# Optimization experiments

Measured on AMD Instinct MI355X. Metric: run time of the kernel, lower is better.

## Reference

```python
import jax, jax.numpy as jnp
import numpy as np

D_IN, L, D, K, N_CLASSES = 1024, 512, 384, 1, 2

def setup_inputs() -> dict:
    key = jax.random.key(0)
    ks = jax.random.split(key, 11)
    x = jax.random.normal(ks[0], (2, 40000, D_IN), dtype=jnp.float32)
    # Linear params stored as [in, out]; xavier-normal-ish scale
    def w(k, i, o):
        return jax.random.normal(k, (i, o), dtype=jnp.float32) * jnp.sqrt(2.0 / (i + o))
    return {
        "x": x,
        "Wf": w(ks[1], D_IN, L), "bf": jnp.zeros((L,), jnp.float32),
        "Wa": w(ks[2], L, D),    "ba": jnp.zeros((D,), jnp.float32),
        "Wb": w(ks[3], L, D),    "bb": jnp.zeros((D,), jnp.float32),
        "Wc": w(ks[4], D, K),    "bc": jnp.zeros((K,), jnp.float32),
        "Wcls": w(ks[5], L * K, N_CLASSES), "bcls": jnp.zeros((N_CLASSES,), jnp.float32),
    }

def reference(x, Wf, bf, Wa, ba, Wb, bb, Wc, bc, Wcls, bcls):
    # feature embed: Linear + ReLU  (mil_norm=None -> Identity norms)
    h = jax.nn.relu(jnp.einsum('bnd,de->bne', x, Wf) + bf)   # [B,N,L]
    # gated attention
    a = jnp.tanh(jnp.einsum('bnl,ld->bnd', h, Wa) + ba)      # [B,N,D]
    g = jax.nn.sigmoid(jnp.einsum('bnl,ld->bnd', h, Wb) + bb)
    s = jnp.einsum('bnd,dk->bnk', a * g, Wc) + bc            # [B,N,K]
    A = jax.nn.softmax(jnp.swapaxes(s, -1, -2), axis=-1)     # [B,K,N]
    pooled = jnp.einsum('bkn,bnl->bkl', A, h)                # [B,K,L]
    logits = jnp.squeeze(pooled, 1) @ Wcls + bcls            # [B,n_classes]
    return logits
```

## Files before the change

kernel.cpp:

```cpp
#include <hip/hip_runtime.h>
#include <cstdint>

typedef _Float16 f16;
typedef __attribute__((ext_vector_type(8))) _Float16 half8;
typedef __attribute__((ext_vector_type(4))) float floatx4;

#define NB      40000
#define M_TOTAL 80000
#define DIN     1024
#define LDIM    512
#define DDIM    384

__global__ void k_prep(const float* __restrict__ Wf, const float* __restrict__ Wa,
                       const float* __restrict__ Wb,
                       f16* __restrict__ packedF, f16* __restrict__ packedAB)
{
    const int gid = blockIdx.x * 256 + threadIdx.x;
    if (gid < 65536) {
        const int lq = gid & 3, n = (gid >> 2) & 511, kb = gid >> 11;
        const int kbase = kb * 32 + lq * 8;
        half8 v;
        #pragma unroll
        for (int j = 0; j < 8; ++j) v[j] = (f16)Wf[(kbase + j) * 512 + n];
        *(half8*)&packedF[(long)gid * 8] = v;
    } else if (gid < 65536 + 49152) {
        const int g = gid - 65536;
        const int kb = g / 3072;
        const int rem = g - kb * 3072;
        const int c = rem >> 2, lq = rem & 3;
        const int d = ((c >> 5) << 4) + (c & 15);
        const int type = (c >> 4) & 1;
        const float* src = type ? Wb : Wa;
        const int kbase = kb * 32 + lq * 8;
        half8 v;
        #pragma unroll
        for (int j = 0; j < 8; ++j) v[j] = (f16)src[(kbase + j) * 384 + d];
        *(half8*)&packedAB[(long)g * 8] = v;
    }
}

__global__ __launch_bounds__(512, 4) void k_gemm1(
    const float* __restrict__ x, const f16* __restrict__ packedF,
    const float* __restrict__ bf, f16* __restrict__ h)
{
    __shared__ __align__(16) f16 As[2][64][72];
    const int tid = threadIdx.x;
    const int w = tid >> 6, lane = tid & 63, lr = lane & 15, lq = lane >> 4;
    const long row0 = (long)blockIdx.x * 64;
    const int sr = tid >> 3, sk = (tid & 7) * 8;
    const float* xp = x + (row0 + sr) * DIN + sk;

    floatx4 acc[4][4] = {};

    float4 xa = *(const float4*)xp;
    float4 xb = *(const float4*)(xp + 4);
    {
        half8 hv;
        hv[0]=(f16)xa.x; hv[1]=(f16)xa.y; hv[2]=(f16)xa.z; hv[3]=(f16)xa.w;
        hv[4]=(f16)xb.x; hv[5]=(f16)xb.y; hv[6]=(f16)xb.z; hv[7]=(f16)xb.w;
        *(half8*)&As[0][sr][sk] = hv;
    }
    for (int kt = 0; kt < 16; ++kt) {
        __syncthreads();
        const int cur = kt & 1;
        if (kt < 15) {
            const float* q = xp + (kt + 1) * 64;
            xa = *(const float4*)q;
            xb = *(const float4*)(q + 4);
        }
        #pragma unroll
        for (int kq = 0; kq < 2; ++kq) {
            const int kb = kt * 2 + kq;
            half8 bfr[4];
            #pragma unroll
            for (int tj = 0; tj < 4; ++tj)
                bfr[tj] = *(const half8*)&packedF[(long)((kb * 512 + w * 64 + tj * 16 + lr) << 5) + lq * 8];
            half8 af[4];
            #pragma unroll
            for (int ti = 0; ti < 4; ++ti)
                af[ti] = *(const half8*)&As[cur][ti * 16 + lr][kq * 32 + lq * 8];
            #pragma unroll
            for (int tj = 0; tj < 4; ++tj)
                #pragma unroll
                for (int ti = 0; ti < 4; ++ti)
                    acc[ti][tj] = __builtin_amdgcn_mfma_f32_16x16x32_f16(af[ti], bfr[tj], acc[ti][tj], 0, 0, 0);
        }
        if (kt < 15) {
            half8 hv;
            hv[0]=(f16)xa.x; hv[1]=(f16)xa.y; hv[2]=(f16)xa.z; hv[3]=(f16)xa.w;
            hv[4]=(f16)xb.x; hv[5]=(f16)xb.y; hv[6]=(f16)xb.z; hv[7]=(f16)xb.w;
            *(half8*)&As[cur ^ 1][sr][sk] = hv;
        }
    }
    #pragma unroll
    for (int tj = 0; tj < 4; ++tj) {
        const int col = w * 64 + tj * 16 + lr;
        const float bias = bf[col];
        #pragma unroll
        for (int ti = 0; ti < 4; ++ti) {
            const long rbase = row0 + ti * 16 + lq * 4;
            #pragma unroll
            for (int r = 0; r < 4; ++r) {
                float v = fmaxf(acc[ti][tj][r] + bias, 0.0f);
                h[(rbase + r) * LDIM + col] = (f16)v;
            }
        }
    }
}

__device__ inline float fast_sigmoid(float xx) { return 1.0f / (1.0f + __expf(-xx)); }
__device__ inline float fast_tanh(float xx) {
    float e = __expf(-2.0f * fabsf(xx));
    float r = (1.0f - e) / (1.0f + e);
    return xx >= 0.0f ? r : -r;
}

__global__ __launch_bounds__(512, 2) void k_gemm2(
    const f16* __restrict__ h, const f16* __restrict__ packedAB,
    const float* __restrict__ ba, const float* __restrict__ bb,
    const float* __restrict__ Wc, float* __restrict__ s)
{
    __shared__ __align__(16) f16 Hs[2][64][136];
    const int tid = threadIdx.x;
    const int w = tid >> 6, lane = tid & 63, lr = lane & 15, lq = lane >> 4;
    const long row0 = (long)blockIdx.x * 64;
    const int sr = tid >> 3, sk = (tid & 7) * 16;
    const f16* hp = h + (row0 + sr) * LDIM + sk;

    floatx4 acc[4][6] = {};

    half8 s0 = *(const half8*)hp;
    half8 s1 = *(const half8*)(hp + 8);
    *(half8*)&Hs[0][sr][sk]     = s0;
    *(half8*)&Hs[0][sr][sk + 8] = s1;

    for (int kt = 0; kt < 4; ++kt) {
        __syncthreads();
        const int cur = kt & 1;
        if (kt < 3) {
            const f16* q = hp + (kt + 1) * 128;
            s0 = *(const half8*)q;
            s1 = *(const half8*)(q + 8);
        }
        #pragma unroll
        for (int kq = 0; kq < 4; ++kq) {
            const int kb = kt * 4 + kq;
            half8 af[4];
            #pragma unroll
            for (int ti = 0; ti < 4; ++ti)
                af[ti] = *(const half8*)&Hs[cur][ti * 16 + lr][kq * 32 + lq * 8];
            #pragma unroll
            for (int tj = 0; tj < 6; ++tj) {
                half8 bfr = *(const half8*)&packedAB[(long)((kb * 768 + w * 96 + tj * 16 + lr) << 5) + lq * 8];
                #pragma unroll
                for (int ti = 0; ti < 4; ++ti)
                    acc[ti][tj] = __builtin_amdgcn_mfma_f32_16x16x32_f16(af[ti], bfr, acc[ti][tj], 0, 0, 0);
            }
        }
        if (kt < 3) {
            *(half8*)&Hs[cur ^ 1][sr][sk]     = s0;
            *(half8*)&Hs[cur ^ 1][sr][sk + 8] = s1;
        }
    }
    float sp[4][4] = {};
    #pragma unroll
    for (int u = 0; u < 3; ++u) {
        const int d = w * 48 + u * 16 + lr;
        const float biasA = ba[d], biasB = bb[d], wcv = Wc[d];
        #pragma unroll
        for (int ti = 0; ti < 4; ++ti)
            #pragma unroll
            for (int r = 0; r < 4; ++r) {
                const float av = fast_tanh(acc[ti][2 * u][r] + biasA);
                const float gv = fast_sigmoid(acc[ti][2 * u + 1][r] + biasB);
                sp[ti][r] += av * gv * wcv;
            }
    }
    #pragma unroll
    for (int m = 1; m < 16; m <<= 1)
        #pragma unroll
        for (int ti = 0; ti < 4; ++ti)
            #pragma unroll
            for (int r = 0; r < 4; ++r)
                sp[ti][r] += __shfl_xor(sp[ti][r], m, 64);
    if (lr == 0) {
        #pragma unroll
        for (int ti = 0; ti < 4; ++ti)
            #pragma unroll
            for (int r = 0; r < 4; ++r)
                atomicAdd(&s[row0 + ti * 16 + lq * 4 + r], sp[ti][r]);
    }
}

__global__ void k_stats(const float* __restrict__ s, float* __restrict__ stats)
{
    const int b = blockIdx.x;
    const int tid = threadIdx.x;
    const float* sb = s + b * NB;
    __shared__ float red[4];
    __shared__ float red2[4];
    __shared__ float smax_sh;
    float m = -3.4e38f;
    for (int i = tid; i < NB; i += 256) m = fmaxf(m, sb[i]);
    #pragma unroll
    for (int o = 32; o > 0; o >>= 1) m = fmaxf(m, __shfl_xor(m, o, 64));
    if ((tid & 63) == 0) red[tid >> 6] = m;
    __syncthreads();
    if (tid == 0) smax_sh = fmaxf(fmaxf(red[0], red[1]), fmaxf(red[2], red[3]));
    __syncthreads();
    const float smax = smax_sh;
    float sum = 0.0f;
    for (int i = tid; i < NB; i += 256) sum += __expf(sb[i] - smax);
    #pragma unroll
    for (int o = 32; o > 0; o >>= 1) sum += __shfl_xor(sum, o, 64);
    if ((tid & 63) == 0) red2[tid >> 6] = sum;
    __syncthreads();
    if (tid == 0) {
        stats[b * 2]     = smax;
        stats[b * 2 + 1] = red2[0] + red2[1] + red2[2] + red2[3];
    }
}

__global__ __launch_bounds__(256) void k_pool(
    const f16* __restrict__ h, const float* __restrict__ s,
    const float* __restrict__ stats, float* __restrict__ pooled)
{
    __shared__ float red[4][512];
    const int bx = blockIdx.x;
    const int b = bx / 250, ch = bx - b * 250;
    const float smax = stats[b * 2];
    const int tid = threadIdx.x;
    const int rg = tid >> 6, cl = (tid & 63) * 8;
    const long nbase = (long)b * NB + ch * 160;
    float a[8] = {};
    for (int r = rg; r < 160; r += 4) {
        const long n = nbase + r;
        const float wgt = __expf(s[n] - smax);
        half8 hv = *(const half8*)&h[n * LDIM + cl];
        #pragma unroll
        for (int j = 0; j < 8; ++j) a[j] += wgt * (float)hv[j];
    }
    #pragma unroll
    for (int j = 0; j < 8; ++j) red[rg][cl + j] = a[j];
    __syncthreads();
    if (rg == 0) {
        #pragma unroll
        for (int j = 0; j < 8; ++j) {
            const int c = cl + j;
            atomicAdd(&pooled[b * LDIM + c], red[0][c] + red[1][c] + red[2][c] + red[3][c]);
        }
    }
}

__global__ void k_logits(const float* __restrict__ pooled, const float* __restrict__ stats,
                         const float* __restrict__ Wcls, const float* __restrict__ bcls,
                         float* __restrict__ out)
{
    const int tid = threadIdx.x;
    const int wave = tid >> 6, lane = tid & 63;
    const int b = wave >> 1, c = wave & 1;
    float sum = 0.0f;
    for (int l = lane; l < LDIM; l += 64)
        sum += pooled[b * LDIM + l] * Wcls[l * 2 + c];
    #pragma unroll
    for (int o = 32; o > 0; o >>= 1) sum += __shfl_xor(sum, o, 64);
    if (lane == 0) out[b * 2 + c] = sum / stats[b * 2 + 1] + bcls[c];
}

extern "C" void kernel_launch(void* const* d_in, const int* in_sizes, int n_in,
                              void* d_out, int out_size, void* d_ws, size_t ws_size,
                              hipStream_t stream)
{
    const float* x    = (const float*)d_in[0];
    const float* Wf   = (const float*)d_in[1];
    const float* bf   = (const float*)d_in[2];
    const float* Wa   = (const float*)d_in[3];
    const float* ba   = (const float*)d_in[4];
    const float* Wb   = (const float*)d_in[5];
    const float* bb   = (const float*)d_in[6];
    const float* Wc   = (const float*)d_in[7];
    const float* Wcls = (const float*)d_in[9];
    const float* bcls = (const float*)d_in[10];
    float* out = (float*)d_out;

    char* w = (char*)d_ws;
    f16*   packedF  = (f16*)(w);
    f16*   packedAB = (f16*)(w + 1048576);
    f16*   hbuf     = (f16*)(w + 1835008);
    float* sbuf     = (float*)(w + 83755008);
    float* stats    = (float*)(w + 84075008);
    float* pooled   = (float*)(w + 84075136);

    hipMemsetAsync(sbuf, 0, 320000, stream);
    hipMemsetAsync(pooled, 0, 4096, stream);

    k_prep  <<<448, 256, 0, stream>>>(Wf, Wa, Wb, packedF, packedAB);
    k_gemm1 <<<M_TOTAL / 64, 512, 0, stream>>>(x, packedF, bf, hbuf);
    k_gemm2 <<<M_TOTAL / 64, 512, 0, stream>>>(hbuf, packedAB, ba, bb, Wc, sbuf);
    k_stats <<<2, 256, 0, stream>>>(sbuf, stats);
    k_pool  <<<500, 256, 0, stream>>>(hbuf, sbuf, stats, pooled);
    k_logits<<<1, 256, 0, stream>>>(pooled, stats, Wcls, bcls, out);
}
```

Before: 824.7 us.

## Fuse both GEMMs, gated attention and pooling into one kernel

Merges the feature GEMM, the gated-attention GEMM, the scoring, the exp-weighting and the per-block pooling into a single kernel. The ReLU activations stay in shared memory, so the large f16 h buffer is never written to or read back from global memory. Softmax is made single-pass by exponentiating scores without subtracting a max, and per-block partial sums are reduced by a small second kernel. This also removes the memsets and several launches. The cost is a large shared-memory footprint per block that lowers occupancy, a single-buffered x tile with an extra barrier per step, and a possible overflow if scores ever grow large.

```diff
diff --git a/kernel.cpp b/kernel.cpp
--- a/kernel.cpp
+++ b/kernel.cpp
@@ -9,7 +9,8 @@
 #define M_TOTAL 80000
 #define DIN     1024
 #define LDIM    512
-#define DDIM    384
+#define NBLK    1250
+#define BPB     625
 
 __global__ void k_prep(const float* __restrict__ Wf, const float* __restrict__ Wa,
                        const float* __restrict__ Wb,
@@ -39,75 +40,6 @@
     }
 }
 
-__global__ __launch_bounds__(512, 4) void k_gemm1(
-    const float* __restrict__ x, const f16* __restrict__ packedF,
-    const float* __restrict__ bf, f16* __restrict__ h)
-{
-    __shared__ __align__(16) f16 As[2][64][72];
-    const int tid = threadIdx.x;
-    const int w = tid >> 6, lane = tid & 63, lr = lane & 15, lq = lane >> 4;
-    const long row0 = (long)blockIdx.x * 64;
-    const int sr = tid >> 3, sk = (tid & 7) * 8;
-    const float* xp = x + (row0 + sr) * DIN + sk;
-
-    floatx4 acc[4][4] = {};
-
-    float4 xa = *(const float4*)xp;
-    float4 xb = *(const float4*)(xp + 4);
-    {
-        half8 hv;
-        hv[0]=(f16)xa.x; hv[1]=(f16)xa.y; hv[2]=(f16)xa.z; hv[3]=(f16)xa.w;
-        hv[4]=(f16)xb.x; hv[5]=(f16)xb.y; hv[6]=(f16)xb.z; hv[7]=(f16)xb.w;
-        *(half8*)&As[0][sr][sk] = hv;
-    }
-    for (int kt = 0; kt < 16; ++kt) {
-        __syncthreads();
-        const int cur = kt & 1;
-        if (kt < 15) {
-            const float* q = xp + (kt + 1) * 64;
-            xa = *(const float4*)q;
-            xb = *(const float4*)(q + 4);
-        }
-        #pragma unroll
-        for (int kq = 0; kq < 2; ++kq) {
-            const int kb = kt * 2 + kq;
-            half8 bfr[4];
-            #pragma unroll
-            for (int tj = 0; tj < 4; ++tj)
-                bfr[tj] = *(const half8*)&packedF[(long)((kb * 512 + w * 64 + tj * 16 + lr) << 5) + lq * 8];
-            half8 af[4];
-            #pragma unroll
-            for (int ti = 0; ti < 4; ++ti)
-                af[ti] = *(const half8*)&As[cur][ti * 16 + lr][kq * 32 + lq * 8];
-            #pragma unroll
-            for (int tj = 0; tj < 4; ++tj)
-                #pragma unroll
-                for (int ti = 0; ti < 4; ++ti)
-                    acc[ti][tj] = __builtin_amdgcn_mfma_f32_16x16x32_f16(af[ti], bfr[tj], acc[ti][tj], 0, 0, 0);
-        }
-        if (kt < 15) {
-            half8 hv;
-            hv[0]=(f16)xa.x; hv[1]=(f16)xa.y; hv[2]=(f16)xa.z; hv[3]=(f16)xa.w;
-            hv[4]=(f16)xb.x; hv[5]=(f16)xb.y; hv[6]=(f16)xb.z; hv[7]=(f16)xb.w;
-            *(half8*)&As[cur ^ 1][sr][sk] = hv;
-        }
-    }
-    #pragma unroll
-    for (int tj = 0; tj < 4; ++tj) {
-        const int col = w * 64 + tj * 16 + lr;
-        const float bias = bf[col];
-        #pragma unroll
-        for (int ti = 0; ti < 4; ++ti) {
-            const long rbase = row0 + ti * 16 + lq * 4;
-            #pragma unroll
-            for (int r = 0; r < 4; ++r) {
-                float v = fmaxf(acc[ti][tj][r] + bias, 0.0f);
-                h[(rbase + r) * LDIM + col] = (f16)v;
-            }
-        }
-    }
-}
-
 __device__ inline float fast_sigmoid(float xx) { return 1.0f / (1.0f + __expf(-xx)); }
 __device__ inline float fast_tanh(float xx) {
     float e = __expf(-2.0f * fabsf(xx));
@@ -115,51 +47,82 @@
     return xx >= 0.0f ? r : -r;
 }
 
-__global__ __launch_bounds__(512, 2) void k_gemm2(
-    const f16* __restrict__ h, const f16* __restrict__ packedAB,
-    const float* __restrict__ ba, const float* __restrict__ bb,
-    const float* __restrict__ Wc, float* __restrict__ s)
-{
-    __shared__ __align__(16) f16 Hs[2][64][136];
+__global__ __launch_bounds__(512, 4) void k_fused(
+    const float* __restrict__ x, const f16* __restrict__ packedF,
+    const f16* __restrict__ packedAB,
+    const float* __restrict__ bf, const float* __restrict__ ba,
+    const float* __restrict__ bb, const float* __restrict__ Wc,
+    float* __restrict__ partial_pool, float* __restrict__ partial_denom)
+{
+    __shared__ __align__(16) f16 Hs[64][520];
+    __shared__ __align__(16) f16 As[64][72];
+    __shared__ float wbuf[64];
     const int tid = threadIdx.x;
     const int w = tid >> 6, lane = tid & 63, lr = lane & 15, lq = lane >> 4;
     const long row0 = (long)blockIdx.x * 64;
-    const int sr = tid >> 3, sk = (tid & 7) * 16;
-    const f16* hp = h + (row0 + sr) * LDIM + sk;
-
-    floatx4 acc[4][6] = {};
-
-    half8 s0 = *(const half8*)hp;
-    half8 s1 = *(const half8*)(hp + 8);
-    *(half8*)&Hs[0][sr][sk]     = s0;
-    *(half8*)&Hs[0][sr][sk + 8] = s1;
-
-    for (int kt = 0; kt < 4; ++kt) {
+    const int sr = tid >> 3, st = (tid & 7) * 8;
+    const float* xp = x + (row0 + sr) * DIN + st;
+    if (tid < 64) wbuf[tid] = 0.0f;
+
+    floatx4 acc[4][4] = {};
+    float4 xa = *(const float4*)xp;
+    float4 xb = *(const float4*)(xp + 4);
+    for (int kt = 0; kt < 16; ++kt) {
         __syncthreads();
-        const int cur = kt & 1;
-        if (kt < 3) {
-            const f16* q = hp + (kt + 1) * 128;
-            s0 = *(const half8*)q;
-            s1 = *(const half8*)(q + 8);
-        }
-        #pragma unroll
-        for (int kq = 0; kq < 4; ++kq) {
-            const int kb = kt * 4 + kq;
+        {
+            half8 hv;
+            hv[0]=(f16)xa.x; hv[1]=(f16)xa.y; hv[2]=(f16)xa.z; hv[3]=(f16)xa.w;
+            hv[4]=(f16)xb.x; hv[5]=(f16)xb.y; hv[6]=(f16)xb.z; hv[7]=(f16)xb.w;
+            *(half8*)&As[sr][st] = hv;
+        }
+        __syncthreads();
+        if (kt < 15) {
+            const float* q = xp + (kt + 1) * 64;
+            xa = *(const float4*)q;
+            xb = *(const float4*)(q + 4);
+        }
+        #pragma unroll
+        for (int kq = 0; kq < 2; ++kq) {
+            const int kb = kt * 2 + kq;
+            half8 bfr[4];
+            #pragma unroll
+            for (int tj = 0; tj < 4; ++tj)
+                bfr[tj] = *(const half8*)&packedF[(long)((kb * 512 + w * 64 + tj * 16 + lr) << 5) + lq * 8];
             half8 af[4];
             #pragma unroll
             for (int ti = 0; ti < 4; ++ti)
-                af[ti] = *(const half8*)&Hs[cur][ti * 16 + lr][kq * 32 + lq * 8];
-            #pragma unroll
-            for (int tj = 0; tj < 6; ++tj) {
-                half8 bfr = *(const half8*)&packedAB[(long)((kb * 768 + w * 96 + tj * 16 + lr) << 5) + lq * 8];
+                af[ti] = *(const half8*)&As[ti * 16 + lr][kq * 32 + lq * 8];
+            #pragma unroll
+            for (int tj = 0; tj < 4; ++tj)
                 #pragma unroll
                 for (int ti = 0; ti < 4; ++ti)
-                    acc[ti][tj] = __builtin_amdgcn_mfma_f32_16x16x32_f16(af[ti], bfr, acc[ti][tj], 0, 0, 0);
-            }
-        }
-        if (kt < 3) {
-            *(half8*)&Hs[cur ^ 1][sr][sk]     = s0;
-            *(half8*)&Hs[cur ^ 1][sr][sk + 8] = s1;
+                    acc[ti][tj] = __builtin_amdgcn_mfma_f32_16x16x32_f16(af[ti], bfr[tj], acc[ti][tj], 0, 0, 0);
+        }
+    }
+    #pragma unroll
+    for (int tj = 0; tj < 4; ++tj) {
+        const int col = w * 64 + tj * 16 + lr;
+        const float bias = bf[col];
+        #pragma unroll
+        for (int ti = 0; ti < 4; ++ti)
+            #pragma unroll
+            for (int r = 0; r < 4; ++r)
+                Hs[ti * 16 + lq * 4 + r][col] = (f16)fmaxf(acc[ti][tj][r] + bias, 0.0f);
+    }
+    __syncthreads();
+
+    floatx4 acc2[4][6] = {};
+    for (int kb = 0; kb < 16; ++kb) {
+        half8 af[4];
+        #pragma unroll
+        for (int ti = 0; ti < 4; ++ti)
+            af[ti] = *(const half8*)&Hs[ti * 16 + lr][kb * 32 + lq * 8];
+        #pragma unroll
+        for (int tj = 0; tj < 6; ++tj) {
+            half8 bfr = *(const half8*)&packedAB[(long)((kb * 768 + w * 96 + tj * 16 + lr) << 5) + lq * 8];
+            #pragma unroll
+            for (int ti = 0; ti < 4; ++ti)
+                acc2[ti][tj] = __builtin_amdgcn_mfma_f32_16x16x32_f16(af[ti], bfr, acc2[ti][tj], 0, 0, 0);
         }
     }
     float sp[4][4] = {};
@@ -171,8 +134,8 @@
         for (int ti = 0; ti < 4; ++ti)
             #pragma unroll
             for (int r = 0; r < 4; ++r) {
-                const float av = fast_tanh(acc[ti][2 * u][r] + biasA);
-                const float gv = fast_sigmoid(acc[ti][2 * u + 1][r] + biasB);
+                const float av = fast_tanh(acc2[ti][2 * u][r] + biasA);
+                const float gv = fast_sigmoid(acc2[ti][2 * u + 1][r] + biasB);
                 sp[ti][r] += av * gv * wcv;
             }
     }
@@ -188,83 +151,57 @@
         for (int ti = 0; ti < 4; ++ti)
             #pragma unroll
             for (int r = 0; r < 4; ++r)
-                atomicAdd(&s[row0 + ti * 16 + lq * 4 + r], sp[ti][r]);
-    }
-}
-
-__global__ void k_stats(const float* __restrict__ s, float* __restrict__ stats)
-{
-    const int b = blockIdx.x;
-    const int tid = threadIdx.x;
-    const float* sb = s + b * NB;
-    __shared__ float red[4];
-    __shared__ float red2[4];
-    __shared__ float smax_sh;
-    float m = -3.4e38f;
-    for (int i = tid; i < NB; i += 256) m = fmaxf(m, sb[i]);
-    #pragma unroll
-    for (int o = 32; o > 0; o >>= 1) m = fmaxf(m, __shfl_xor(m, o, 64));
-    if ((tid & 63) == 0) red[tid >> 6] = m;
-    __syncthreads();
-    if (tid == 0) smax_sh = fmaxf(fmaxf(red[0], red[1]), fmaxf(red[2], red[3]));
-    __syncthreads();
-    const float smax = smax_sh;
-    float sum = 0.0f;
-    for (int i = tid; i < NB; i += 256) sum += __expf(sb[i] - smax);
-    #pragma unroll
-    for (int o = 32; o > 0; o >>= 1) sum += __shfl_xor(sum, o, 64);
-    if ((tid & 63) == 0) red2[tid >> 6] = sum;
-    __syncthreads();
-    if (tid == 0) {
-        stats[b * 2]     = smax;
-        stats[b * 2 + 1] = red2[0] + red2[1] + red2[2] + red2[3];
-    }
-}
-
-__global__ __launch_bounds__(256) void k_pool(
-    const f16* __restrict__ h, const float* __restrict__ s,
-    const float* __restrict__ stats, float* __restrict__ pooled)
-{
-    __shared__ float red[4][512];
-    const int bx = blockIdx.x;
-    const int b = bx / 250, ch = bx - b * 250;
-    const float smax = stats[b * 2];
-    const int tid = threadIdx.x;
-    const int rg = tid >> 6, cl = (tid & 63) * 8;
-    const long nbase = (long)b * NB + ch * 160;
-    float a[8] = {};
-    for (int r = rg; r < 160; r += 4) {
-        const long n = nbase + r;
-        const float wgt = __expf(s[n] - smax);
-        half8 hv = *(const half8*)&h[n * LDIM + cl];
-        #pragma unroll
-        for (int j = 0; j < 8; ++j) a[j] += wgt * (float)hv[j];
-    }
-    #pragma unroll
-    for (int j = 0; j < 8; ++j) red[rg][cl + j] = a[j];
-    __syncthreads();
-    if (rg == 0) {
-        #pragma unroll
-        for (int j = 0; j < 8; ++j) {
-            const int c = cl + j;
-            atomicAdd(&pooled[b * LDIM + c], red[0][c] + red[1][c] + red[2][c] + red[3][c]);
-        }
-    }
-}
-
-__global__ void k_logits(const float* __restrict__ pooled, const float* __restrict__ stats,
-                         const float* __restrict__ Wcls, const float* __restrict__ bcls,
-                         float* __restrict__ out)
-{
-    const int tid = threadIdx.x;
-    const int wave = tid >> 6, lane = tid & 63;
-    const int b = wave >> 1, c = wave & 1;
-    float sum = 0.0f;
-    for (int l = lane; l < LDIM; l += 64)
-        sum += pooled[b * LDIM + l] * Wcls[l * 2 + c];
-    #pragma unroll
-    for (int o = 32; o > 0; o >>= 1) sum += __shfl_xor(sum, o, 64);
-    if (lane == 0) out[b * 2 + c] = sum / stats[b * 2 + 1] + bcls[c];
+                atomicAdd(&wbuf[ti * 16 + lq * 4 + r], sp[ti][r]);
+    }
+    __syncthreads();
+    if (tid < 64) wbuf[tid] = __expf(wbuf[tid]);
+    __syncthreads();
+
+    {
+        const int c = tid;
+        float pacc = 0.0f;
+        #pragma unroll 8
+        for (int n = 0; n < 64; ++n)
+            pacc += wbuf[n] * (float)Hs[n][c];
+        partial_pool[(long)blockIdx.x * 512 + c] = pacc;
+    }
+    if (w == 0) {
+        float dsum = wbuf[lane];
+        #pragma unroll
+        for (int o = 32; o > 0; o >>= 1) dsum += __shfl_xor(dsum, o, 64);
+        if (lane == 0) partial_denom[blockIdx.x] = dsum;
+    }
+}
+
+__global__ __launch_bounds__(512) void k_reduce(
+    const float* __restrict__ pp, const float* __restrict__ pd,
+    const float* __restrict__ Wcls, const float* __restrict__ bcls,
+    float* __restrict__ out)
+{
+    __shared__ float pooled[512];
+    __shared__ float dsh[8];
+    const int b = blockIdx.x, tid = threadIdx.x;
+    float acc = 0.0f;
+    const float* base = pp + (long)b * BPB * 512 + tid;
+    for (int i = 0; i < BPB; ++i) acc += base[(long)i * 512];
+    pooled[tid] = acc;
+    float d = 0.0f;
+    for (int i = tid; i < BPB; i += 512) d += pd[b * BPB + i];
+    #pragma unroll
+    for (int o = 32; o > 0; o >>= 1) d += __shfl_xor(d, o, 64);
+    if ((tid & 63) == 0) dsh[tid >> 6] = d;
+    __syncthreads();
+    const float denom = dsh[0] + dsh[1] + dsh[2] + dsh[3] + dsh[4] + dsh[5] + dsh[6] + dsh[7];
+    if (tid < 128) {
+        const int cls = tid >> 6, ln = tid & 63;
+        float sum = 0.0f;
+        #pragma unroll
+        for (int t = 0; t < 8; ++t)
+            sum += pooled[t * 64 + ln] * Wcls[(t * 64 + ln) * 2 + cls];
+        #pragma unroll
+        for (int o = 32; o > 0; o >>= 1) sum += __shfl_xor(sum, o, 64);
+        if (ln == 0) out[b * 2 + cls] = sum / denom + bcls[cls];
+    }
 }
 
 extern "C" void kernel_launch(void* const* d_in, const int* in_sizes, int n_in,
@@ -286,18 +223,10 @@
     char* w = (char*)d_ws;
     f16*   packedF  = (f16*)(w);
     f16*   packedAB = (f16*)(w + 1048576);
-    f16*   hbuf     = (f16*)(w + 1835008);
-    float* sbuf     = (float*)(w + 83755008);
-    float* stats    = (float*)(w + 84075008);
-    float* pooled   = (float*)(w + 84075136);
-
-    hipMemsetAsync(sbuf, 0, 320000, stream);
-    hipMemsetAsync(pooled, 0, 4096, stream);
+    float* ppool    = (float*)(w + 1835008);
+    float* pdenom   = (float*)(w + 4395008);
 
     k_prep  <<<448, 256, 0, stream>>>(Wf, Wa, Wb, packedF, packedAB);
-    k_gemm1 <<<M_TOTAL / 64, 512, 0, stream>>>(x, packedF, bf, hbuf);
-    k_gemm2 <<<M_TOTAL / 64, 512, 0, stream>>>(hbuf, packedAB, ba, bb, Wc, sbuf);
-    k_stats <<<2, 256, 0, stream>>>(sbuf, stats);
-    k_pool  <<<500, 256, 0, stream>>>(hbuf, sbuf, stats, pooled);
-    k_logits<<<1, 256, 0, stream>>>(pooled, stats, Wcls, bcls, out);
-}
+    k_fused <<<NBLK, 512, 0, stream>>>(x, packedF, packedAB, bf, ba, bb, Wc, ppool, pdenom);
+    k_reduce<<<2, 512, 0, stream>>>(ppool, pdenom, Wcls, bcls, out);
+}
```

New measurement: 717.2 us. 13.0% less time.
